# Kernel tuning notes

Hardware: AMD Instinct MI355X
Metric: run time of the kernel (lower is better)

Reference implementation:

```python
import jax, jax.numpy as jnp
import numpy as np

N_NODES = 50000
N_EDGES = 800000
IN_F = 128
OUT_F = 128
N_LAYERS = 2


def setup_inputs() -> dict:
    key = jax.random.key(0)
    ks = jax.random.split(key, 8)
    x = jax.random.normal(ks[0], (N_NODES, IN_F), dtype=jnp.float32)
    hidden_states = jax.random.normal(ks[1], (N_LAYERS, N_NODES, OUT_F), dtype=jnp.float32)
    src = jax.random.randint(ks[2], (N_EDGES,), 0, N_NODES)
    dst = jax.random.randint(ks[3], (N_EDGES,), 0, N_NODES)
    edge_w = jax.random.uniform(ks[4], (N_EDGES,), dtype=jnp.float32)
    # [layer, gate(r,u,c), in+out, out], scaled like typical init
    W_self = jax.random.normal(ks[5], (N_LAYERS, 3, IN_F + OUT_F, OUT_F), dtype=jnp.float32) * 0.05
    W_neigh = jax.random.normal(ks[6], (N_LAYERS, 3, IN_F + OUT_F, OUT_F), dtype=jnp.float32) * 0.05
    bias = jax.random.uniform(ks[7], (N_LAYERS, 3, OUT_F), dtype=jnp.float32)
    return {"x": x, "hidden_states": hidden_states, "src": src, "dst": dst,
            "edge_w": edge_w, "W_self": W_self, "W_neigh": W_neigh, "bias": bias}


def _gconv(z, src, dst, edge_w, ws, wn):
    # z: [N, 2F]; message passing: sum_{e: dst=v} edge_w[e] * z[src[e]]
    msg = z[src] * edge_w[:, None]                      # [E, 2F]
    agg = jax.ops.segment_sum(msg, dst, num_segments=N_NODES)  # [N, 2F]
    return z @ ws + agg @ wn                            # [N, F]


def _cell(x, h, src, dst, edge_w, ws, wn, b):
    # ws/wn: [3, 2F, F], b: [3, F]; gates r,u,c as in GraphGRUCell
    xh = jnp.concatenate([x, h], axis=1)
    r = jax.nn.sigmoid(_gconv(xh, src, dst, edge_w, ws[0], wn[0]) + b[0])
    u = jax.nn.sigmoid(_gconv(xh, src, dst, edge_w, ws[1], wn[1]) + b[1])
    xh2 = jnp.concatenate([x, r * h], axis=1)
    c = jax.nn.sigmoid(_gconv(xh2, src, dst, edge_w, ws[2], wn[2]) + b[2])
    return u * h + (1.0 - u) * c


def reference(x, hidden_states, src, dst, edge_w, W_self, W_neigh, bias):
    hiddens = []
    for i in range(N_LAYERS):  # small fixed layer count
        x = _cell(x, hidden_states[i], src, dst, edge_w, W_self[i], W_neigh[i], bias[i])
        hiddens.append(x)
    return (x, hiddens)
```

## Files before the change

### kernel.cpp

```cpp
#include <hip/hip_runtime.h>
#include <math.h>

#define F 128
#define NLAYERS 2

typedef __attribute__((ext_vector_type(8))) short bf16x8s;
typedef __attribute__((ext_vector_type(8))) unsigned short u16x8;
typedef __attribute__((ext_vector_type(4))) float f32x4;

__device__ __forceinline__ float sigmoidf_(float x) { return 1.0f / (1.0f + expf(-x)); }

__device__ __forceinline__ unsigned short f2bf(float f) {
    unsigned int u = __float_as_uint(f);
    u += 0x7fffu + ((u >> 16) & 1u);
    return (unsigned short)(u >> 16);
}
__device__ __forceinline__ float bf2f(unsigned short s) {
    return __uint_as_float(((unsigned int)s) << 16);
}

__global__ void pack_w_bf16(const float* __restrict__ Ws, const float* __restrict__ Wn,
                            unsigned short* __restrict__ W1b, unsigned short* __restrict__ W2b) {
    int t = blockIdx.x * blockDim.x + threadIdx.x;
    const int n1 = 2 * 64 * 256 * 8;
    if (t < n1) {
        int j = t & 7, n = (t >> 3) & 255, ko = (t >> 11) & 63, l = t >> 17;
        int k = ko * 8 + j;
        int p = k >> 7, r = k & 127, g = n >> 7, c = n & 127;
        const float* W = (p < 2) ? Ws : Wn;
        W1b[t] = f2bf(W[(((l * 3 + g) * 256) + ((p & 1) * 128 + r)) * 128 + c]);
    } else {
        int t2 = t - n1;
        if (t2 >= 2 * 64 * 128 * 8) return;
        int j = t2 & 7, n = (t2 >> 3) & 127, ko = (t2 >> 10) & 63, l = t2 >> 16;
        int k = ko * 8 + j;
        int p = k >> 7, r = k & 127;
        const float* W = (p < 2) ? Ws : Wn;
        W2b[t2] = f2bf(W[(((l * 3 + 2) * 256) + ((p & 1) * 128 + r)) * 128 + n]);
    }
}

__global__ void cvt_bf16_i(const float* __restrict__ in, unsigned short* __restrict__ out, int n4) {
    int t = blockIdx.x * blockDim.x + threadIdx.x;
    if (t >= n4) return;
    float4 v = reinterpret_cast<const float4*>(in)[t];
    ushort4 o;
    o.x = f2bf(v.x); o.y = f2bf(v.y); o.z = f2bf(v.z); o.w = f2bf(v.w);
    *reinterpret_cast<ushort4*>(out + (((size_t)(t >> 5)) << 8) + ((t & 31) << 2)) = o;
}

__global__ void hist_dst(const int* __restrict__ dst, int* __restrict__ cnt, int E) {
    int e = blockIdx.x * blockDim.x + threadIdx.x;
    if (e < E) atomicAdd(&cnt[dst[e]], 1);
}

__global__ __launch_bounds__(1024) void scan_blk(const int* __restrict__ cnt,
                                                 int* __restrict__ offs,
                                                 int* __restrict__ bsum, int n) {
    __shared__ int wsum[16];
    int tid = threadIdx.x, lane = tid & 63, wid = tid >> 6;
    int i = blockIdx.x * 1024 + tid;
    int v = (i < n) ? cnt[i] : 0;
    int incl = v;
#pragma unroll
    for (int off = 1; off < 64; off <<= 1) {
        int t = __shfl_up(incl, off, 64);
        if (lane >= off) incl += t;
    }
    if (lane == 63) wsum[wid] = incl;
    __syncthreads();
    if (wid == 0) {
        int s = (lane < 16) ? wsum[lane] : 0;
#pragma unroll
        for (int off = 1; off < 16; off <<= 1) {
            int t = __shfl_up(s, off, 64);
            if (lane >= off) s += t;
        }
        if (lane < 16) wsum[lane] = s;
    }
    __syncthreads();
    int wbase = (wid > 0) ? wsum[wid - 1] : 0;
    if (i < n) offs[i] = wbase + incl - v;
    if (tid == 1023) bsum[blockIdx.x] = wbase + incl;
}

__global__ __launch_bounds__(1024) void scan_tops(int* __restrict__ bsum, int nb,
                                                  int* __restrict__ total_out) {
    __shared__ int wsum[16];
    int tid = threadIdx.x, lane = tid & 63, wid = tid >> 6;
    int v = (tid < nb) ? bsum[tid] : 0;
    int incl = v;
#pragma unroll
    for (int off = 1; off < 64; off <<= 1) {
        int t = __shfl_up(incl, off, 64);
        if (lane >= off) incl += t;
    }
    if (lane == 63) wsum[wid] = incl;
    __syncthreads();
    if (wid == 0) {
        int s = (lane < 16) ? wsum[lane] : 0;
#pragma unroll
        for (int off = 1; off < 16; off <<= 1) {
            int t = __shfl_up(s, off, 64);
            if (lane >= off) s += t;
        }
        if (lane < 16) wsum[lane] = s;
    }
    __syncthreads();
    int wbase = (wid > 0) ? wsum[wid - 1] : 0;
    if (tid < nb) bsum[tid] = wbase + incl - v;
    if (tid == 1023) *total_out = wbase + incl;
}

__global__ __launch_bounds__(1024) void scan_add(const int* __restrict__ bsum,
                                                 int* __restrict__ offs,
                                                 int* __restrict__ cursor, int n) {
    int i = blockIdx.x * 1024 + threadIdx.x;
    if (i >= n) return;
    int o = offs[i] + bsum[blockIdx.x];
    offs[i] = o;
    cursor[i] = o;
}

__global__ void scatter_edges(const int* __restrict__ src, const int* __restrict__ dst,
                              const float* __restrict__ ew, int* __restrict__ cursor,
                              int2* __restrict__ es, int E) {
    int e = blockIdx.x * blockDim.x + threadIdx.x;
    if (e >= E) return;
    int d = dst[e];
    int p = atomicAdd(&cursor[d], 1);
    es[p] = make_int2(src[e], __float_as_int(ew[e]));
}

__global__ __launch_bounds__(256) void agg_csr2_i(
    const unsigned short* __restrict__ XH,
    const int2* __restrict__ es, const int* __restrict__ offs,
    unsigned short* __restrict__ agg0, unsigned short* __restrict__ agg1, int N) {
    int node = blockIdx.x * 8 + (threadIdx.x >> 5);
    if (node >= N) return;
    int lane = threadIdx.x & 31;
    int beg = offs[node], end = offs[node + 1];
    float a0[8] = {0, 0, 0, 0, 0, 0, 0, 0};
    float a1[8] = {0, 0, 0, 0, 0, 0, 0, 0};
    int loff = lane << 3;
    int i = beg;
    for (; i + 3 < end; i += 4) {
        int2 e0 = es[i], e1 = es[i + 1], e2 = es[i + 2], e3 = es[i + 3];
        u16x8 v0 = *reinterpret_cast<const u16x8*>(XH + (((size_t)e0.x) << 8) + loff);
        u16x8 v1 = *reinterpret_cast<const u16x8*>(XH + (((size_t)e1.x) << 8) + loff);
        u16x8 v2 = *reinterpret_cast<const u16x8*>(XH + (((size_t)e2.x) << 8) + loff);
        u16x8 v3 = *reinterpret_cast<const u16x8*>(XH + (((size_t)e3.x) << 8) + loff);
        float w0 = __int_as_float(e0.y), w1 = __int_as_float(e1.y);
        float w2 = __int_as_float(e2.y), w3 = __int_as_float(e3.y);
#pragma unroll
        for (int j = 0; j < 8; ++j) {
            a0[j] += w0 * bf2f(v0[j]);
            a1[j] += w1 * bf2f(v1[j]);
            a0[j] += w2 * bf2f(v2[j]);
            a1[j] += w3 * bf2f(v3[j]);
        }
    }
    for (; i < end; ++i) {
        int2 e0 = es[i];
        float w0 = __int_as_float(e0.y);
        u16x8 v0 = *reinterpret_cast<const u16x8*>(XH + (((size_t)e0.x) << 8) + loff);
#pragma unroll
        for (int j = 0; j < 8; ++j) a0[j] += w0 * bf2f(v0[j]);
    }
    u16x8 o;
#pragma unroll
    for (int j = 0; j < 8; ++j) o[j] = f2bf(a0[j] + a1[j]);
    unsigned short* op = (lane < 16)
        ? (agg0 + (((size_t)node) << 7) + (lane << 3))
        : (agg1 + (((size_t)node) << 7) + ((lane & 15) << 3));
    *reinterpret_cast<u16x8*>(op) = o;
}

__global__ __launch_bounds__(256) void agg_csr1_b(
    const unsigned short* __restrict__ V0,
    const int2* __restrict__ es, const int* __restrict__ offs,
    unsigned short* __restrict__ agg0, int N) {
    int node = blockIdx.x * 8 + (threadIdx.x >> 5);
    if (node >= N) return;
    int lane = threadIdx.x & 31;
    int beg = offs[node], end = offs[node + 1];
    float p0[4] = {0, 0, 0, 0}, p1[4] = {0, 0, 0, 0};
    int loff = lane << 2;
    int i = beg;
    for (; i + 3 < end; i += 4) {
        int2 e0 = es[i], e1 = es[i + 1], e2 = es[i + 2], e3 = es[i + 3];
        ushort4 x0 = *reinterpret_cast<const ushort4*>(V0 + (((size_t)e0.x) << 7) + loff);
        ushort4 x1 = *reinterpret_cast<const ushort4*>(V0 + (((size_t)e1.x) << 7) + loff);
        ushort4 x2 = *reinterpret_cast<const ushort4*>(V0 + (((size_t)e2.x) << 7) + loff);
        ushort4 x3 = *reinterpret_cast<const ushort4*>(V0 + (((size_t)e3.x) << 7) + loff);
        float w0 = __int_as_float(e0.y), w1 = __int_as_float(e1.y);
        float w2 = __int_as_float(e2.y), w3 = __int_as_float(e3.y);
        p0[0] += w0 * bf2f(x0.x); p0[1] += w0 * bf2f(x0.y);
        p0[2] += w0 * bf2f(x0.z); p0[3] += w0 * bf2f(x0.w);
        p1[0] += w1 * bf2f(x1.x); p1[1] += w1 * bf2f(x1.y);
        p1[2] += w1 * bf2f(x1.z); p1[3] += w1 * bf2f(x1.w);
        p0[0] += w2 * bf2f(x2.x); p0[1] += w2 * bf2f(x2.y);
        p0[2] += w2 * bf2f(x2.z); p0[3] += w2 * bf2f(x2.w);
        p1[0] += w3 * bf2f(x3.x); p1[1] += w3 * bf2f(x3.y);
        p1[2] += w3 * bf2f(x3.z); p1[3] += w3 * bf2f(x3.w);
    }
    for (; i < end; ++i) {
        int2 e0 = es[i];
        float w0 = __int_as_float(e0.y);
        ushort4 x0 = *reinterpret_cast<const ushort4*>(V0 + (((size_t)e0.x) << 7) + loff);
        p0[0] += w0 * bf2f(x0.x); p0[1] += w0 * bf2f(x0.y);
        p0[2] += w0 * bf2f(x0.z); p0[3] += w0 * bf2f(x0.w);
    }
    size_t ob = (((size_t)node) << 7) + loff;
    ushort4 o0;
    o0.x = f2bf(p0[0] + p1[0]); o0.y = f2bf(p0[1] + p1[1]);
    o0.z = f2bf(p0[2] + p1[2]); o0.w = f2bf(p0[3] + p1[3]);
    *reinterpret_cast<ushort4*>(agg0 + ob) = o0;
}

__global__ __launch_bounds__(256) void gemm_mfma(
    const unsigned short* __restrict__ A0, const unsigned short* __restrict__ A1,
    const unsigned short* __restrict__ A2, const unsigned short* __restrict__ A3,
    int sA0, int sA1, int obsh,
    const unsigned short* __restrict__ Wb, const float* __restrict__ bias,
    const float* __restrict__ hfull, const float* __restrict__ uin,
    unsigned short* __restrict__ outb, float* __restrict__ outf,
    float* __restrict__ outf2, int Nn, int Ntot, int mode) {
    __shared__ __align__(16) unsigned short Als[2][4 * 64 * 8];
    __shared__ __align__(16) unsigned short Bls[2][4 * 128 * 8];
    const unsigned short* parts[4] = {A0, A1, A2, A3};

    int tid = threadIdx.x;
    int row0 = blockIdx.x * 64;
    int n0c = blockIdx.y * 128;
    int lane = tid & 63;
    int w = tid >> 6;
    int wrow = (w & 1) << 5;
    int wcol = (w >> 1) << 6;
    int quad = lane >> 4, l16 = lane & 15;

    f32x4 acc[2][4];
    const f32x4 z4 = {0.f, 0.f, 0.f, 0.f};
#pragma unroll
    for (int mt = 0; mt < 2; ++mt)
#pragma unroll
        for (int nt = 0; nt < 4; ++nt) acc[mt][nt] = z4;

    int growA = row0 + lane;
    if (growA >= Nn) growA = Nn - 1;
    int qB = tid >> 7, nB = tid & 127;

    auto stage = [&](int ks, int buf) {
        int p = ks >> 7;
        size_t roff = (p == 0) ? (size_t)growA * (size_t)sA0
                    : (p == 1) ? (size_t)growA * (size_t)sA1
                               : ((size_t)growA << 7);
        const unsigned short* ga = parts[p] + roff + (ks & 127) + (w << 3);
        __builtin_amdgcn_global_load_lds(
            (const __attribute__((address_space(1))) void*)ga,
            (__attribute__((address_space(3))) void*)&Als[buf][((w << 6) + lane) << 3], 16, 0, 0);
#pragma unroll
        for (int r = 0; r < 2; ++r) {
            int q = 2 * r + qB;
            int koG = (ks >> 3) + q;
            const unsigned short* gb = Wb + ((size_t)(koG * Ntot + n0c + nB) << 3);
            __builtin_amdgcn_global_load_lds(
                (const __attribute__((address_space(1))) void*)gb,
                (__attribute__((address_space(3))) void*)&Bls[buf][((q << 7) + nB) << 3], 16, 0, 0);
        }
    };

    stage(0, 0);
    __syncthreads();
    int buf = 0;
    for (int ks = 0; ks < 512; ks += 32, buf ^= 1) {
        if (ks + 32 < 512) stage(ks + 32, buf ^ 1);

        bf16x8s af[2], bfr[4];
#pragma unroll
        for (int mt = 0; mt < 2; ++mt)
            af[mt] = *reinterpret_cast<const bf16x8s*>(
                &Als[buf][((quad << 6) + wrow + (mt << 4) + l16) << 3]);
#pragma unroll
        for (int nt = 0; nt < 4; ++nt)
            bfr[nt] = *reinterpret_cast<const bf16x8s*>(
                &Bls[buf][((quad << 7) + wcol + (nt << 4) + l16) << 3]);
#pragma unroll
        for (int mt = 0; mt < 2; ++mt)
#pragma unroll
            for (int nt = 0; nt < 4; ++nt)
                acc[mt][nt] = __builtin_amdgcn_mfma_f32_16x16x32_bf16(
                    af[mt], bfr[nt], acc[mt][nt], 0, 0, 0);
        __syncthreads();
    }

#pragma unroll
    for (int mt = 0; mt < 2; ++mt) {
#pragma unroll
        for (int reg = 0; reg < 4; ++reg) {
            int row = row0 + wrow + (mt << 4) + (quad << 2) + reg;
            if (row >= Nn) continue;
#pragma unroll
            for (int nt = 0; nt < 4; ++nt) {
                int col = n0c + wcol + (nt << 4) + l16;
                float val = acc[mt][nt][reg] + bias[col];
                if (mode == 0) {
                    float sg = sigmoidf_(val);
                    int c = col & 127;
                    size_t o = ((size_t)row << 7) + c;
                    if (col < 128)
                        outb[o] = f2bf(sg * hfull[o]);
                    else
                        outf[o] = sg;
                } else {
                    float cv = sigmoidf_(val);
                    size_t o = ((size_t)row << 7) + col;
                    float uu = uin[o];
                    float hh = hfull[o];
                    float hn = uu * hh + (1.0f - uu) * cv;
                    outf[o] = hn;
                    if (outf2) outf2[o] = hn;
                    outb[((size_t)row << obsh) + col] = f2bf(hn);
                }
            }
        }
    }
}

extern "C" void kernel_launch(void* const* d_in, const int* in_sizes, int n_in,
                              void* d_out, int out_size, void* d_ws, size_t ws_size,
                              hipStream_t stream) {
    const float* x      = (const float*)d_in[0];
    const float* hidden = (const float*)d_in[1];
    const int*   src    = (const int*)d_in[2];
    const int*   dst    = (const int*)d_in[3];
    const float* ew     = (const float*)d_in[4];
    const float* Wself  = (const float*)d_in[5];
    const float* Wneigh = (const float*)d_in[6];
    const float* bias   = (const float*)d_in[7];
    float* out = (float*)d_out;

    int N = in_sizes[0] / F;
    int E = in_sizes[2];
    size_t NF = (size_t)N * F;

    char* p = (char*)d_ws;
    auto alloc = [&](size_t bytes) { char* r = p; p += (bytes + 255) & ~255ull; return r; };
    unsigned short* xh0    = (unsigned short*)alloc(2 * NF * 2);
    unsigned short* xh1    = (unsigned short*)alloc(2 * NF * 2);
    unsigned short* agg_xb = (unsigned short*)alloc(NF * 2);
    unsigned short* agg_hb = (unsigned short*)alloc(NF * 2);
    unsigned short* agg_rb = (unsigned short*)alloc(NF * 2);
    unsigned short* rhb    = (unsigned short*)alloc(NF * 2);
    float*          u      = (float*)alloc(NF * 4);
    unsigned short* W1b    = (unsigned short*)alloc(2 * 64 * 256 * 8 * 2);
    unsigned short* W2b    = (unsigned short*)alloc(2 * 64 * 128 * 8 * 2);
    int2*           es     = (int2*)alloc((size_t)E * 8);
    int*            cnt    = (int*)alloc((size_t)N * 4);
    int*            offs   = (int*)alloc(((size_t)N + 1) * 4);
    int*            cursor = (int*)alloc((size_t)N * 4);
    int*            bsum   = (int*)alloc(1024 * 4);

    pack_w_bf16<<<dim3(1536), dim3(256), 0, stream>>>(Wself, Wneigh, W1b, W2b);
    int n4 = (int)(NF / 4);
    int cblk = (n4 + 255) / 256;
    cvt_bf16_i<<<dim3(cblk), dim3(256), 0, stream>>>(x, xh0, n4);
    cvt_bf16_i<<<dim3(cblk), dim3(256), 0, stream>>>(hidden, xh0 + 128, n4);
    cvt_bf16_i<<<dim3(cblk), dim3(256), 0, stream>>>(hidden + NF, xh1 + 128, n4);

    hipMemsetAsync(cnt, 0, (size_t)N * sizeof(int), stream);
    int eBlocks = (E + 255) / 256;
    hist_dst<<<dim3(eBlocks), dim3(256), 0, stream>>>(dst, cnt, E);
    int nb = (N + 1023) / 1024;
    scan_blk<<<dim3(nb), dim3(1024), 0, stream>>>(cnt, offs, bsum, N);
    scan_tops<<<dim3(1), dim3(1024), 0, stream>>>(bsum, nb, offs + N);
    scan_add<<<dim3(nb), dim3(1024), 0, stream>>>(bsum, offs, cursor, N);
    scatter_edges<<<dim3(eBlocks), dim3(256), 0, stream>>>(src, dst, ew, cursor, es, E);

    float* out_x  = out;
    float* out_h1 = out + NF;
    float* out_h2 = out + 2 * NF;

    int aggBlocks = (N + 7) / 8;
    int mBlocks = (N + 63) / 64;
    for (int l = 0; l < NLAYERS; ++l) {
        unsigned short* xhL = (l == 0) ? xh0 : xh1;
        const float* hL = hidden + (size_t)l * NF;
        const float* biasL = bias + (size_t)l * 384;

        agg_csr2_i<<<dim3(aggBlocks), dim3(256), 0, stream>>>(xhL, es, offs,
                                                              agg_xb, agg_hb, N);

        gemm_mfma<<<dim3(mBlocks, 2), dim3(256), 0, stream>>>(
            xhL, xhL + 128, agg_xb, agg_hb, 256, 256, 7,
            W1b + (size_t)l * 64 * 256 * 8, biasL, hL, nullptr,
            rhb, u, nullptr, N, 256, 0);

        agg_csr1_b<<<dim3(aggBlocks), dim3(256), 0, stream>>>(rhb, es, offs, agg_rb, N);

        float* o1 = (l == 0) ? out_h1 : out_h2;
        float* o2 = (l == NLAYERS - 1) ? out_x : nullptr;
        unsigned short* obN = (l == 0) ? xh1 : agg_rb;
        int obsh = (l == 0) ? 8 : 7;
        gemm_mfma<<<dim3(mBlocks, 1), dim3(256), 0, stream>>>(
            xhL, rhb, agg_xb, agg_rb, 256, 128, obsh,
            W2b + (size_t)l * 64 * 128 * 8, biasL + 256, hL, u,
            obN, o1, o2, N, 128, 1);
    }
}
```

Before: 608.5 us.

## Sort CSR edges by source bucket, fuse conversions, split GEMM into r/u and c kernels

New measurement: 633.6 us. 1.04x slower.

```diff
diff --git a/kernel.cpp b/kernel.cpp
--- a/kernel.cpp
+++ b/kernel.cpp
@@ -40,18 +40,27 @@
     }
 }
 
-__global__ void cvt_bf16_i(const float* __restrict__ in, unsigned short* __restrict__ out, int n4) {
+__global__ void cvt_all(const float* __restrict__ x, const float* __restrict__ hidden,
+                        unsigned short* __restrict__ xh0, unsigned short* __restrict__ xh1,
+                        int n4, size_t NF) {
     int t = blockIdx.x * blockDim.x + threadIdx.x;
-    if (t >= n4) return;
-    float4 v = reinterpret_cast<const float4*>(in)[t];
+    const float* in;
+    unsigned short* out;
+    int tt;
+    if (t < n4) { in = x; out = xh0; tt = t; }
+    else if (t < 2 * n4) { in = hidden; out = xh0 + 128; tt = t - n4; }
+    else if (t < 3 * n4) { in = hidden + NF; out = xh1 + 128; tt = t - 2 * n4; }
+    else return;
+    float4 v = reinterpret_cast<const float4*>(in)[tt];
     ushort4 o;
     o.x = f2bf(v.x); o.y = f2bf(v.y); o.z = f2bf(v.z); o.w = f2bf(v.w);
-    *reinterpret_cast<ushort4*>(out + (((size_t)(t >> 5)) << 8) + ((t & 31) << 2)) = o;
-}
-
-__global__ void hist_dst(const int* __restrict__ dst, int* __restrict__ cnt, int E) {
+    *reinterpret_cast<ushort4*>(out + (((size_t)(tt >> 5)) << 8) + ((tt & 31) << 2)) = o;
+}
+
+__global__ void hist_key(const int* __restrict__ src, const int* __restrict__ dst,
+                         int* __restrict__ cnt, int E) {
     int e = blockIdx.x * blockDim.x + threadIdx.x;
-    if (e < E) atomicAdd(&cnt[dst[e]], 1);
+    if (e < E) atomicAdd(&cnt[(dst[e] << 4) + (src[e] >> 12)], 1);
 }
 
 __global__ __launch_bounds__(1024) void scan_blk(const int* __restrict__ cnt,
@@ -127,19 +136,20 @@
                               int2* __restrict__ es, int E) {
     int e = blockIdx.x * blockDim.x + threadIdx.x;
     if (e >= E) return;
-    int d = dst[e];
-    int p = atomicAdd(&cursor[d], 1);
-    es[p] = make_int2(src[e], __float_as_int(ew[e]));
+    int s = src[e];
+    int key = (dst[e] << 4) + (s >> 12);
+    int p = atomicAdd(&cursor[key], 1);
+    es[p] = make_int2(s, __float_as_int(ew[e]));
 }
 
 __global__ __launch_bounds__(256) void agg_csr2_i(
     const unsigned short* __restrict__ XH,
-    const int2* __restrict__ es, const int* __restrict__ offs,
+    const int2* __restrict__ es, const int* __restrict__ offs2,
     unsigned short* __restrict__ agg0, unsigned short* __restrict__ agg1, int N) {
     int node = blockIdx.x * 8 + (threadIdx.x >> 5);
     if (node >= N) return;
     int lane = threadIdx.x & 31;
-    int beg = offs[node], end = offs[node + 1];
+    int beg = offs2[node << 4], end = offs2[(node << 4) + 16];
     float a0[8] = {0, 0, 0, 0, 0, 0, 0, 0};
     float a1[8] = {0, 0, 0, 0, 0, 0, 0, 0};
     int loff = lane << 3;
@@ -178,12 +188,12 @@
 
 __global__ __launch_bounds__(256) void agg_csr1_b(
     const unsigned short* __restrict__ V0,
-    const int2* __restrict__ es, const int* __restrict__ offs,
+    const int2* __restrict__ es, const int* __restrict__ offs2,
     unsigned short* __restrict__ agg0, int N) {
     int node = blockIdx.x * 8 + (threadIdx.x >> 5);
     if (node >= N) return;
     int lane = threadIdx.x & 31;
-    int beg = offs[node], end = offs[node + 1];
+    int beg = offs2[node << 4], end = offs2[(node << 4) + 16];
     float p0[4] = {0, 0, 0, 0}, p1[4] = {0, 0, 0, 0};
     int loff = lane << 2;
     int i = beg;
@@ -218,21 +228,112 @@
     *reinterpret_cast<ushort4*>(agg0 + ob) = o0;
 }
 
-__global__ __launch_bounds__(256) void gemm_mfma(
-    const unsigned short* __restrict__ A0, const unsigned short* __restrict__ A1,
-    const unsigned short* __restrict__ A2, const unsigned short* __restrict__ A3,
-    int sA0, int sA1, int obsh,
+__global__ __launch_bounds__(256) void gemm_ru(
+    const unsigned short* __restrict__ XH,
+    const unsigned short* __restrict__ AGGX, const unsigned short* __restrict__ AGGH,
+    const unsigned short* __restrict__ Wb, const float* __restrict__ bias,
+    const float* __restrict__ hfull,
+    unsigned short* __restrict__ rhb, float* __restrict__ u, int N) {
+    __shared__ __align__(16) unsigned short Als[2][4 * 64 * 8];
+    __shared__ __align__(16) unsigned short Bls[2][4 * 256 * 8];
+
+    int tid = threadIdx.x;
+    int row0 = blockIdx.x * 64;
+    int lane = tid & 63;
+    int w = tid >> 6;
+    int wrow = (w & 1) << 5;
+    int wcol = (w >> 1) << 7;
+    int quad = lane >> 4, l16 = lane & 15;
+
+    f32x4 acc[2][8];
+    const f32x4 z4 = {0.f, 0.f, 0.f, 0.f};
+#pragma unroll
+    for (int mt = 0; mt < 2; ++mt)
+#pragma unroll
+        for (int nt = 0; nt < 8; ++nt) acc[mt][nt] = z4;
+
+    int growA = row0 + lane;
+    if (growA >= N) growA = N - 1;
+
+    auto stage = [&](int ks, int buf) {
+        int p = ks >> 7;
+        const unsigned short* ga =
+            (p == 0) ? (XH + (size_t)growA * 256 + (ks & 127) + (w << 3))
+          : (p == 1) ? (XH + (size_t)growA * 256 + 128 + (ks & 127) + (w << 3))
+          : (p == 2) ? (AGGX + ((size_t)growA << 7) + (ks & 127) + (w << 3))
+                     : (AGGH + ((size_t)growA << 7) + (ks & 127) + (w << 3));
+        __builtin_amdgcn_global_load_lds(
+            (const __attribute__((address_space(1))) void*)ga,
+            (__attribute__((address_space(3))) void*)&Als[buf][((w << 6) + lane) << 3], 16, 0, 0);
+#pragma unroll
+        for (int r = 0; r < 4; ++r) {
+            int q = r, n = tid;
+            int koG = (ks >> 3) + q;
+            const unsigned short* gb = Wb + ((size_t)(koG * 256 + n) << 3);
+            __builtin_amdgcn_global_load_lds(
+                (const __attribute__((address_space(1))) void*)gb,
+                (__attribute__((address_space(3))) void*)&Bls[buf][((q << 8) + n) << 3], 16, 0, 0);
+        }
+    };
+
+    stage(0, 0);
+    __syncthreads();
+    int buf = 0;
+    for (int ks = 0; ks < 512; ks += 32, buf ^= 1) {
+        if (ks + 32 < 512) stage(ks + 32, buf ^ 1);
+
+        bf16x8s af[2], bfr[8];
+#pragma unroll
+        for (int mt = 0; mt < 2; ++mt)
+            af[mt] = *reinterpret_cast<const bf16x8s*>(
+                &Als[buf][((quad << 6) + wrow + (mt << 4) + l16) << 3]);
+#pragma unroll
+        for (int nt = 0; nt < 8; ++nt)
+            bfr[nt] = *reinterpret_cast<const bf16x8s*>(
+                &Bls[buf][((quad << 8) + wcol + (nt << 4) + l16) << 3]);
+#pragma unroll
+        for (int mt = 0; mt < 2; ++mt)
+#pragma unroll
+            for (int nt = 0; nt < 8; ++nt)
+                acc[mt][nt] = __builtin_amdgcn_mfma_f32_16x16x32_bf16(
+                    af[mt], bfr[nt], acc[mt][nt], 0, 0, 0);
+        __syncthreads();
+    }
+
+#pragma unroll
+    for (int mt = 0; mt < 2; ++mt) {
+#pragma unroll
+        for (int reg = 0; reg < 4; ++reg) {
+            int row = row0 + wrow + (mt << 4) + (quad << 2) + reg;
+            if (row >= N) continue;
+#pragma unroll
+            for (int nt = 0; nt < 8; ++nt) {
+                int col = wcol + (nt << 4) + l16;
+                float val = acc[mt][nt][reg] + bias[col];
+                float sg = sigmoidf_(val);
+                int c = col & 127;
+                size_t o = ((size_t)row << 7) + c;
+                if (col < 128)
+                    rhb[o] = f2bf(sg * hfull[o]);
+                else
+                    u[o] = sg;
+            }
+        }
+    }
+}
+
+__global__ __launch_bounds__(256) void gemm_c(
+    const unsigned short* __restrict__ XH, const unsigned short* __restrict__ RHB,
+    const unsigned short* __restrict__ AGGX, const unsigned short* __restrict__ AGGR,
     const unsigned short* __restrict__ Wb, const float* __restrict__ bias,
     const float* __restrict__ hfull, const float* __restrict__ uin,
     unsigned short* __restrict__ outb, float* __restrict__ outf,
-    float* __restrict__ outf2, int Nn, int Ntot, int mode) {
+    float* __restrict__ outf2, int obsh, int N) {
     __shared__ __align__(16) unsigned short Als[2][4 * 64 * 8];
     __shared__ __align__(16) unsigned short Bls[2][4 * 128 * 8];
-    const unsigned short* parts[4] = {A0, A1, A2, A3};
 
     int tid = threadIdx.x;
     int row0 = blockIdx.x * 64;
-    int n0c = blockIdx.y * 128;
     int lane = tid & 63;
     int w = tid >> 6;
     int wrow = (w & 1) << 5;
@@ -247,15 +348,16 @@
         for (int nt = 0; nt < 4; ++nt) acc[mt][nt] = z4;
 
     int growA = row0 + lane;
-    if (growA >= Nn) growA = Nn - 1;
+    if (growA >= N) growA = N - 1;
     int qB = tid >> 7, nB = tid & 127;
 
     auto stage = [&](int ks, int buf) {
         int p = ks >> 7;
-        size_t roff = (p == 0) ? (size_t)growA * (size_t)sA0
-                    : (p == 1) ? (size_t)growA * (size_t)sA1
-                               : ((size_t)growA << 7);
-        const unsigned short* ga = parts[p] + roff + (ks & 127) + (w << 3);
+        const unsigned short* ga =
+            (p == 0) ? (XH + (size_t)growA * 256 + (ks & 127) + (w << 3))
+          : (p == 1) ? (RHB + ((size_t)growA << 7) + (ks & 127) + (w << 3))
+          : (p == 2) ? (AGGX + ((size_t)growA << 7) + (ks & 127) + (w << 3))
+                     : (AGGR + ((size_t)growA << 7) + (ks & 127) + (w << 3));
         __builtin_amdgcn_global_load_lds(
             (const __attribute__((address_space(1))) void*)ga,
             (__attribute__((address_space(3))) void*)&Als[buf][((w << 6) + lane) << 3], 16, 0, 0);
@@ -263,7 +365,7 @@
         for (int r = 0; r < 2; ++r) {
             int q = 2 * r + qB;
             int koG = (ks >> 3) + q;
-            const unsigned short* gb = Wb + ((size_t)(koG * Ntot + n0c + nB) << 3);
+            const unsigned short* gb = Wb + ((size_t)(koG * 128 + nB) << 3);
             __builtin_amdgcn_global_load_lds(
                 (const __attribute__((address_space(1))) void*)gb,
                 (__attribute__((address_space(3))) void*)&Bls[buf][((q << 7) + nB) << 3], 16, 0, 0);
@@ -299,29 +401,19 @@
 #pragma unroll
         for (int reg = 0; reg < 4; ++reg) {
             int row = row0 + wrow + (mt << 4) + (quad << 2) + reg;
-            if (row >= Nn) continue;
+            if (row >= N) continue;
 #pragma unroll
             for (int nt = 0; nt < 4; ++nt) {
-                int col = n0c + wcol + (nt << 4) + l16;
+                int col = wcol + (nt << 4) + l16;
                 float val = acc[mt][nt][reg] + bias[col];
-                if (mode == 0) {
-                    float sg = sigmoidf_(val);
-                    int c = col & 127;
-                    size_t o = ((size_t)row << 7) + c;
-                    if (col < 128)
-                        outb[o] = f2bf(sg * hfull[o]);
-                    else
-                        outf[o] = sg;
-                } else {
-                    float cv = sigmoidf_(val);
-                    size_t o = ((size_t)row << 7) + col;
-                    float uu = uin[o];
-                    float hh = hfull[o];
-                    float hn = uu * hh + (1.0f - uu) * cv;
-                    outf[o] = hn;
-                    if (outf2) outf2[o] = hn;
-                    outb[((size_t)row << obsh) + col] = f2bf(hn);
-                }
+                float cv = sigmoidf_(val);
+                size_t o = ((size_t)row << 7) + col;
+                float uu = uin[o];
+                float hh = hfull[o];
+                float hn = uu * hh + (1.0f - uu) * cv;
+                outf[o] = hn;
+                if (outf2) outf2[o] = hn;
+                outb[((size_t)row << obsh) + col] = f2bf(hn);
             }
         }
     }
@@ -343,6 +435,7 @@
     int N = in_sizes[0] / F;
     int E = in_sizes[2];
     size_t NF = (size_t)N * F;
+    int NK = N * 16;
 
     char* p = (char*)d_ws;
     auto alloc = [&](size_t bytes) { char* r = p; p += (bytes + 255) & ~255ull; return r; };
@@ -356,26 +449,23 @@
     unsigned short* W1b    = (unsigned short*)alloc(2 * 64 * 256 * 8 * 2);
     unsigned short* W2b    = (unsigned short*)alloc(2 * 64 * 128 * 8 * 2);
     int2*           es     = (int2*)alloc((size_t)E * 8);
-    int*            cnt    = (int*)alloc((size_t)N * 4);
-    int*            offs   = (int*)alloc(((size_t)N + 1) * 4);
-    int*            cursor = (int*)alloc((size_t)N * 4);
+    int*            cnt2   = (int*)alloc((size_t)NK * 4);
+    int*            offs2  = (int*)alloc(((size_t)NK + 1) * 4);
+    int*            cur2   = (int*)alloc((size_t)NK * 4);
     int*            bsum   = (int*)alloc(1024 * 4);
 
     pack_w_bf16<<<dim3(1536), dim3(256), 0, stream>>>(Wself, Wneigh, W1b, W2b);
     int n4 = (int)(NF / 4);
-    int cblk = (n4 + 255) / 256;
-    cvt_bf16_i<<<dim3(cblk), dim3(256), 0, stream>>>(x, xh0, n4);
-    cvt_bf16_i<<<dim3(cblk), dim3(256), 0, stream>>>(hidden, xh0 + 128, n4);
-    cvt_bf16_i<<<dim3(cblk), dim3(256), 0, stream>>>(hidden + NF, xh1 + 128, n4);
-
-    hipMemsetAsync(cnt, 0, (size_t)N * sizeof(int), stream);
+    cvt_all<<<dim3((3 * n4 + 255) / 256), dim3(256), 0, stream>>>(x, hidden, xh0, xh1, n4, NF);
+
+    hipMemsetAsync(cnt2, 0, (size_t)NK * sizeof(int), stream);
     int eBlocks = (E + 255) / 256;
-    hist_dst<<<dim3(eBlocks), dim3(256), 0, stream>>>(dst, cnt, E);
-    int nb = (N + 1023) / 1024;
-    scan_blk<<<dim3(nb), dim3(1024), 0, stream>>>(cnt, offs, bsum, N);
-    scan_tops<<<dim3(1), dim3(1024), 0, stream>>>(bsum, nb, offs + N);
-    scan_add<<<dim3(nb), dim3(1024), 0, stream>>>(bsum, offs, cursor, N);
-    scatter_edges<<<dim3(eBlocks), dim3(256), 0, stream>>>(src, dst, ew, cursor, es, E);
+    hist_key<<<dim3(eBlocks), dim3(256), 0, stream>>>(src, dst, cnt2, E);
+    int nb = (NK + 1023) / 1024;
+    scan_blk<<<dim3(nb), dim3(1024), 0, stream>>>(cnt2, offs2, bsum, NK);
+    scan_tops<<<dim3(1), dim3(1024), 0, stream>>>(bsum, nb, offs2 + NK);
+    scan_add<<<dim3(nb), dim3(1024), 0, stream>>>(bsum, offs2, cur2, NK);
+    scatter_edges<<<dim3(eBlocks), dim3(256), 0, stream>>>(src, dst, ew, cur2, es, E);
 
     float* out_x  = out;
     float* out_h1 = out + NF;
@@ -388,23 +478,23 @@
         const float* hL = hidden + (size_t)l * NF;
         const float* biasL = bias + (size_t)l * 384;
 
-        agg_csr2_i<<<dim3(aggBlocks), dim3(256), 0, stream>>>(xhL, es, offs,
+        agg_csr2_i<<<dim3(aggBlocks), dim3(256), 0, stream>>>(xhL, es, offs2,
                                                               agg_xb, agg_hb, N);
 
-        gemm_mfma<<<dim3(mBlocks, 2), dim3(256), 0, stream>>>(
-            xhL, xhL + 128, agg_xb, agg_hb, 256, 256, 7,
-            W1b + (size_t)l * 64 * 256 * 8, biasL, hL, nullptr,
-            rhb, u, nullptr, N, 256, 0);
-
-        agg_csr1_b<<<dim3(aggBlocks), dim3(256), 0, stream>>>(rhb, es, offs, agg_rb, N);
+        gemm_ru<<<dim3(mBlocks), dim3(256), 0, stream>>>(
+            xhL, agg_xb, agg_hb,
+            W1b + (size_t)l * 64 * 256 * 8, biasL, hL,
+            rhb, u, N);
+
+        agg_csr1_b<<<dim3(aggBlocks), dim3(256), 0, stream>>>(rhb, es, offs2, agg_rb, N);
 
         float* o1 = (l == 0) ? out_h1 : out_h2;
         float* o2 = (l == NLAYERS - 1) ? out_x : nullptr;
         unsigned short* obN = (l == 0) ? xh1 : agg_rb;
         int obsh = (l == 0) ? 8 : 7;
-        gemm_mfma<<<dim3(mBlocks, 1), dim3(256), 0, stream>>>(
-            xhL, rhb, agg_xb, agg_rb, 256, 128, obsh,
+        gemm_c<<<dim3(mBlocks), dim3(256), 0, stream>>>(
+            xhL, rhb, agg_xb, agg_rb,
             W2b + (size_t)l * 64 * 128 * 8, biasL + 256, hL, u,
-            obN, o1, o2, N, 128, 1);
-    }
-}
+            obN, o1, o2, obsh, N);
+    }
+}
```
